# Kernel optimization log

Measured on AMD Instinct MI355X. Metric: run time of the kernel, lower is better.

Reference implementation:

```python
import jax, jax.numpy as jnp
import numpy as np

DIM, HEADS, DHEAD, CTX_DIM, FF_MULT = 320, 8, 40, 768, 4
INNER_FF = FF_MULT * DIM  # 1280
EPS = 1e-5


def layer_norm(x, g, b):
    mu = jnp.mean(x, axis=-1, keepdims=True)
    var = jnp.mean((x - mu) ** 2, axis=-1, keepdims=True)
    return (x - mu) * jax.lax.rsqrt(var + EPS) * g + b


def attention(x, ctx, wq, wk, wv, wo, bo):
    # x: [b, i, DIM], ctx: [b, j, c]
    b, i, _ = x.shape
    j = ctx.shape[1]
    q = (x @ wq).reshape(b, i, HEADS, DHEAD)
    k = (ctx @ wk).reshape(b, j, HEADS, DHEAD)
    v = (ctx @ wv).reshape(b, j, HEADS, DHEAD)
    scale = DHEAD ** -0.5
    sim = jnp.einsum('bihd,bjhd->bhij', q, k) * scale  # full NxN, non-flash
    attn = jax.nn.softmax(sim, axis=-1)
    out = jnp.einsum('bhij,bjhd->bihd', attn, v).reshape(b, i, HEADS * DHEAD)
    return out @ wo + bo


def setup_inputs() -> dict:
    key = jax.random.key(0)
    ks = jax.random.split(key, 24)
    nrm = lambda k, shp, fan: jax.random.normal(k, shp, jnp.float32) * (fan ** -0.5)
    d = {
        'x': jax.random.normal(ks[0], (1, 4096, DIM), jnp.float32),
        'context': jax.random.normal(ks[1], (1, 77, CTX_DIM), jnp.float32),
        'n1_g': jnp.ones((DIM,), jnp.float32), 'n1_b': jnp.zeros((DIM,), jnp.float32),
        'a1_wq': nrm(ks[2], (DIM, DIM), DIM), 'a1_wk': nrm(ks[3], (DIM, DIM), DIM),
        'a1_wv': nrm(ks[4], (DIM, DIM), DIM), 'a1_wo': nrm(ks[5], (DIM, DIM), DIM),
        'a1_bo': jnp.zeros((DIM,), jnp.float32),
        'n2_g': jnp.ones((DIM,), jnp.float32), 'n2_b': jnp.zeros((DIM,), jnp.float32),
        'a2_wq': nrm(ks[6], (DIM, DIM), DIM), 'a2_wk': nrm(ks[7], (CTX_DIM, DIM), CTX_DIM),
        'a2_wv': nrm(ks[8], (CTX_DIM, DIM), CTX_DIM), 'a2_wo': nrm(ks[9], (DIM, DIM), DIM),
        'a2_bo': jnp.zeros((DIM,), jnp.float32),
        'n3_g': jnp.ones((DIM,), jnp.float32), 'n3_b': jnp.zeros((DIM,), jnp.float32),
        'ff_w1': nrm(ks[10], (DIM, 2 * INNER_FF), DIM),
        'ff_b1': jnp.zeros((2 * INNER_FF,), jnp.float32),
        'ff_w2': nrm(ks[11], (INNER_FF, DIM), INNER_FF),
        'ff_b2': jnp.zeros((DIM,), jnp.float32),
    }
    return d


def reference(x, context, n1_g, n1_b, a1_wq, a1_wk, a1_wv, a1_wo, a1_bo,
              n2_g, n2_b, a2_wq, a2_wk, a2_wv, a2_wo, a2_bo,
              n3_g, n3_b, ff_w1, ff_b1, ff_w2, ff_b2):
    # self-attention
    x = attention(layer_norm(x, n1_g, n1_b), layer_norm(x, n1_g, n1_b),
                  a1_wq, a1_wk, a1_wv, a1_wo, a1_bo) + x
    # cross-attention with text context
    x = attention(layer_norm(x, n2_g, n2_b), context,
                  a2_wq, a2_wk, a2_wv, a2_wo, a2_bo) + x
    # GEGLU feed-forward
    h = layer_norm(x, n3_g, n3_b) @ ff_w1 + ff_b1
    val, gate = jnp.split(h, 2, axis=-1)
    x = (val * jax.nn.gelu(gate, approximate=False)) @ ff_w2 + ff_b2 + x
    return x
```

## Files before the change

kernel.cpp:

```cpp
#include <hip/hip_runtime.h>
#include <hip/hip_bf16.h>
#include <math.h>

typedef __bf16 bf16;
typedef __attribute__((ext_vector_type(8))) __bf16 bf16x8;
typedef __attribute__((ext_vector_type(4))) __bf16 bf16x4;
typedef __attribute__((ext_vector_type(4))) float f32x4;
typedef __attribute__((ext_vector_type(2))) float f32x2;
typedef __attribute__((ext_vector_type(4))) short shortx4;

#define NTOK 4096
#define DIM  320
#define HEADS 8
#define DHEAD 40
#define NCTX 77
#define CTXD 768
#define IFF  1280

#define QSCALE (0.15811388300841897f * 1.4426950408889634f)

__device__ __forceinline__ bf16x8 bzero8() {
    bf16x8 v;
#pragma unroll
    for (int e = 0; e < 8; ++e) v[e] = (bf16)0.0f;
    return v;
}

__device__ __forceinline__ void gld_lds16(const void* g, void* l) {
    __builtin_amdgcn_global_load_lds(
        (const __attribute__((address_space(1))) void*)g,
        (__attribute__((address_space(3))) void*)l, 16, 0, 0);
}

#define PRE_TILES 2280
#define CONV_BLOCKS 231

struct PreJob { const float* src; bf16* dst; int K, N, ntx, tile0, perm; };
struct PreTab { PreJob j[10]; };

__global__ __launch_bounds__(256)
void preprocess_all(PreTab P, const float* __restrict__ ctx, bf16* __restrict__ ctxb) {
    const int b = blockIdx.x;
    const int tx = threadIdx.x, ty = threadIdx.y;
    if (b >= PRE_TILES) {
        int i = (b - PRE_TILES) * 256 + ty * 32 + tx;
        if (i < NCTX * CTXD) ctxb[i] = (bf16)ctx[i];
        return;
    }
    int ji = 0;
#pragma unroll
    for (int k = 1; k < 10; ++k)
        if (b >= P.j[k].tile0) ji = k;
    const PreJob jb = P.j[ji];
    const int local = b - jb.tile0;
    const int n0 = (local % jb.ntx) * 32;
    const int k0 = (local / jb.ntx) * 32;

    __shared__ float tile[32][33];
#pragma unroll
    for (int i = 0; i < 4; ++i)
        tile[ty + i * 8][tx] = jb.src[(size_t)(k0 + ty + i * 8) * jb.N + n0 + tx];
    __syncthreads();
#pragma unroll
    for (int i = 0; i < 4; ++i) {
        int n = n0 + ty + i * 8;
        int nd = jb.perm ? ((n < 1280) ? 2 * n : 2 * (n - 1280) + 1) : n;
        jb.dst[(size_t)nd * jb.K + k0 + tx] = (bf16)tile[tx][ty + i * 8];
    }
}

__global__ __launch_bounds__(256)
void layernorm_kernel(const float* __restrict__ X, const float* __restrict__ g,
                      const float* __restrict__ b, bf16* __restrict__ Y) {
    int w = threadIdx.x >> 6, lane = threadIdx.x & 63;
    int row = blockIdx.x * 4 + w;
    const float* xr = X + (size_t)row * DIM;
    float v[5];
    float sum = 0.f;
#pragma unroll
    for (int c = 0; c < 5; ++c) { v[c] = xr[c * 64 + lane]; sum += v[c]; }
#pragma unroll
    for (int off = 1; off < 64; off <<= 1) sum += __shfl_xor(sum, off);
    float mu = sum * (1.f / 320.f);
    float vs = 0.f;
#pragma unroll
    for (int c = 0; c < 5; ++c) { float d = v[c] - mu; vs += d * d; }
#pragma unroll
    for (int off = 1; off < 64; off <<= 1) vs += __shfl_xor(vs, off);
    float rs = rsqrtf(vs * (1.f / 320.f) + 1e-5f);
    bf16* yr = Y + (size_t)row * DIM;
#pragma unroll
    for (int c = 0; c < 5; ++c)
        yr[c * 64 + lane] = (bf16)((v[c] - mu) * rs * g[c * 64 + lane] + b[c * 64 + lane]);
}

template <int EPI, int BM, int BN>
__global__ __launch_bounds__(256)
void gemm_db(const bf16* __restrict__ A, const bf16* __restrict__ Bt,
             int M, int N, int K,
             bf16* __restrict__ Y0, bf16* __restrict__ Y1, bf16* __restrict__ Y2,
             float* Yf, const float* __restrict__ bias, const float* res, int trs) {
    constexpr int ABYTES = BM * 128;
    constexpr int BBYTES = BN * 128;
    constexpr int FB = ABYTES + BBYTES;
    constexpr int WM = BM / 2;
    constexpr int WN = BN / 2;
    constexpr int MI = WM / 16;
    constexpr int NI = WN / 16;
    constexpr int ACH = BM / 32;
    constexpr int BCH = BN / 32;
    __shared__ char smem[2 * FB];
    const int t = threadIdx.x, lane = t & 63, w = t >> 6;
    const int wr = w >> 1, wc = w & 1;
    const int m0 = blockIdx.x * BM;
    const int n0 = blockIdx.y * BN;

    const bf16* asrc[ACH];
    const bf16* bsrc[BCH];
#pragma unroll
    for (int i = 0; i < ACH; ++i) {
        int ch = i * 256 + t;
        int row = ch >> 3, seg = (ch & 7) ^ (row & 7);
        asrc[i] = A + (size_t)(m0 + row) * K + seg * 8;
    }
#pragma unroll
    for (int i = 0; i < BCH; ++i) {
        int ch = i * 256 + t;
        int row = ch >> 3, seg = (ch & 7) ^ (row & 7);
        bsrc[i] = Bt + (size_t)(n0 + row) * K + seg * 8;
    }

    f32x4 acc[MI][NI];
#pragma unroll
    for (int mi = 0; mi < MI; ++mi)
#pragma unroll
        for (int ni = 0; ni < NI; ++ni)
#pragma unroll
            for (int r = 0; r < 4; ++r) acc[mi][ni][r] = 0.f;

    auto STAGE = [&](char* base, int k0) {
#pragma unroll
        for (int i = 0; i < ACH; ++i)
            gld_lds16(asrc[i] + k0, base + (i * 256 + w * 64) * 16);
#pragma unroll
        for (int i = 0; i < BCH; ++i)
            gld_lds16(bsrc[i] + k0, base + ABYTES + (i * 256 + w * 64) * 16);
    };

    char* cur = smem;
    char* nxt = smem + FB;
    STAGE(cur, 0);
    __syncthreads();

    for (int k0 = 0; k0 < K; k0 += 64) {
        if (k0 + 64 < K) STAGE(nxt, k0 + 64);
        bf16x8 a[MI][2], b[NI][2];
#pragma unroll
        for (int mi = 0; mi < MI; ++mi)
#pragma unroll
            for (int kh = 0; kh < 2; ++kh) {
                int row = wr * WM + mi * 16 + (lane & 15);
                a[mi][kh] = *(const bf16x8*)(cur + row * 128 +
                             ((kh * 64 + (lane >> 4) * 16) ^ ((row & 7) << 4)));
            }
#pragma unroll
        for (int ni = 0; ni < NI; ++ni)
#pragma unroll
            for (int kh = 0; kh < 2; ++kh) {
                int row = wc * WN + ni * 16 + (lane & 15);
                b[ni][kh] = *(const bf16x8*)(cur + ABYTES + row * 128 +
                             ((kh * 64 + (lane >> 4) * 16) ^ ((row & 7) << 4)));
            }
#pragma unroll
        for (int mi = 0; mi < MI; ++mi)
#pragma unroll
            for (int ni = 0; ni < NI; ++ni) {
                acc[mi][ni] = __builtin_amdgcn_mfma_f32_16x16x32_bf16(a[mi][0], b[ni][0], acc[mi][ni], 0, 0, 0);
                acc[mi][ni] = __builtin_amdgcn_mfma_f32_16x16x32_bf16(a[mi][1], b[ni][1], acc[mi][ni], 0, 0, 0);
            }
        __syncthreads();
        char* tmp = cur; cur = nxt; nxt = tmp;
    }

#pragma unroll
    for (int mi = 0; mi < MI; ++mi)
#pragma unroll
        for (int ni = 0; ni < NI; ++ni) {
            const int col = n0 + wc * WN + ni * 16 + (lane & 15);
            const int rowb = m0 + wr * WM + mi * 16 + (lane >> 4) * 4;
            if (EPI == 5) {
                if (col < 320) {
#pragma unroll
                    for (int r = 0; r < 4; ++r)
                        Y0[(size_t)(rowb + r) * 320 + col] = (bf16)(acc[mi][ni][r] * QSCALE);
                } else if (col < 640) {
#pragma unroll
                    for (int r = 0; r < 4; ++r)
                        Y1[(size_t)(rowb + r) * 320 + (col - 320)] = (bf16)acc[mi][ni][r];
                } else {
                    bf16x4 tv;
#pragma unroll
                    for (int r = 0; r < 4; ++r) tv[r] = (bf16)acc[mi][ni][r];
                    *(bf16x4*)(Y2 + (size_t)(col - 640) * trs + rowb) = tv;
                }
            } else if (EPI == 7) {
                int bidx = (col & 1) ? (1280 + (col >> 1)) : (col >> 1);
                float bc = bias[bidx];
#pragma unroll
                for (int r = 0; r < 4; ++r) {
                    float v = acc[mi][ni][r] + bc;
                    float other = __shfl_xor(v, 1);
                    if (!(col & 1)) {
                        float gl = 0.5f * other * (1.f + erff(other * 0.70710678118654752f));
                        Y0[(size_t)(rowb + r) * 1280 + (col >> 1)] = (bf16)(v * gl);
                    }
                }
            } else {
#pragma unroll
                for (int r = 0; r < 4; ++r) {
                    int row = rowb + r;
                    if (row < M) {
                        float v = acc[mi][ni][r];
                        if (EPI == 4) Y0[(size_t)row * N + col] = (bf16)(v * QSCALE);
                        else Yf[(size_t)row * N + col] = v + bias[col] + res[(size_t)row * N + col];
                    }
                }
            }
        }
}

__global__ __launch_bounds__(256)
void gemm_small6(const bf16* __restrict__ A, const bf16* __restrict__ Bt,
                 int M, int N, int K,
                 bf16* __restrict__ Y0, bf16* __restrict__ Y2, int trs) {
    __shared__ char smem[24 * 1024];
    const int t = threadIdx.x;
    const int lane = t & 63;
    const int w = t >> 6;
    const int wr = w >> 1, wc = w & 1;
    const int m0 = 0;
    const int n0 = blockIdx.y * 64;

    f32x4 acc[4][2];
#pragma unroll
    for (int mi = 0; mi < 4; ++mi)
#pragma unroll
        for (int ni = 0; ni < 2; ++ni)
#pragma unroll
            for (int r = 0; r < 4; ++r) acc[mi][ni][r] = 0.f;

    for (int k0 = 0; k0 < K; k0 += 64) {
#pragma unroll
        for (int i = 0; i < 4; ++i) {
            int c = t + i * 256;
            int row = c >> 3, seg = c & 7;
            int gr = m0 + row;
            bf16x8 v = bzero8();
            if (gr < M) v = *(const bf16x8*)(A + (size_t)gr * K + k0 + seg * 8);
            *(bf16x8*)(smem + row * 128 + ((seg * 16) ^ ((row & 7) << 4))) = v;
        }
#pragma unroll
        for (int i = 0; i < 2; ++i) {
            int c = t + i * 256;
            int row = c >> 3, seg = c & 7;
            bf16x8 v = *(const bf16x8*)(Bt + (size_t)(n0 + row) * K + k0 + seg * 8);
            *(bf16x8*)(smem + 16 * 1024 + row * 128 + ((seg * 16) ^ ((row & 7) << 4))) = v;
        }
        __syncthreads();

        bf16x8 a[4][2], bfr[2][2];
#pragma unroll
        for (int mi = 0; mi < 4; ++mi)
#pragma unroll
            for (int kh = 0; kh < 2; ++kh) {
                int row = wr * 64 + mi * 16 + (lane & 15);
                a[mi][kh] = *(const bf16x8*)(smem + row * 128 +
                             ((kh * 64 + (lane >> 4) * 16) ^ ((row & 7) << 4)));
            }
#pragma unroll
        for (int ni = 0; ni < 2; ++ni)
#pragma unroll
            for (int kh = 0; kh < 2; ++kh) {
                int row = wc * 32 + ni * 16 + (lane & 15);
                bfr[ni][kh] = *(const bf16x8*)(smem + 16 * 1024 + row * 128 +
                               ((kh * 64 + (lane >> 4) * 16) ^ ((row & 7) << 4)));
            }
#pragma unroll
        for (int mi = 0; mi < 4; ++mi)
#pragma unroll
            for (int ni = 0; ni < 2; ++ni) {
                acc[mi][ni] = __builtin_amdgcn_mfma_f32_16x16x32_bf16(a[mi][0], bfr[ni][0], acc[mi][ni], 0, 0, 0);
                acc[mi][ni] = __builtin_amdgcn_mfma_f32_16x16x32_bf16(a[mi][1], bfr[ni][1], acc[mi][ni], 0, 0, 0);
            }
        __syncthreads();
    }

#pragma unroll
    for (int mi = 0; mi < 4; ++mi)
#pragma unroll
        for (int ni = 0; ni < 2; ++ni) {
            const int col = n0 + wc * 32 + ni * 16 + (lane & 15);
            const int rowb = m0 + wr * 64 + mi * 16 + (lane >> 4) * 4;
            if (col < 320) {
#pragma unroll
                for (int r = 0; r < 4; ++r)
                    if (rowb + r < M) Y0[(size_t)(rowb + r) * 320 + col] = (bf16)acc[mi][ni][r];
            } else {
                bf16x4 tv;
#pragma unroll
                for (int r = 0; r < 4; ++r) tv[r] = (bf16)acc[mi][ni][r];
                *(bf16x4*)(Y2 + (size_t)(col - 320) * trs + rowb) = tv;
            }
        }
}

#define KVT 64
#define KBYTES 5120
#define VBYTES 6144
#define FBUF (KBYTES + VBYTES)

template <int DIRECT>
__global__ __launch_bounds__(256, 4)
void flash_attn5(const bf16* __restrict__ Qg, const bf16* __restrict__ Kg,
                 const bf16* __restrict__ VTg, bf16* __restrict__ O,
                 float* __restrict__ Opart, float* __restrict__ MLpart,
                 int nkv, int vstride, int tiles_per_split) {
    __shared__ char smem[2 * FBUF];
    const int t = threadIdx.x, lane = t & 63, w = t >> 6;
    const int g = lane >> 4, q = lane & 15;
    const int h = blockIdx.y, split = blockIdx.z;
    const int qb = blockIdx.x * 64 + w * 16;

    const int ntiles = (nkv + KVT - 1) / KVT;
    const int tt0 = split * tiles_per_split;
    int tt1 = tt0 + tiles_per_split;
    if (tt1 > ntiles) tt1 = ntiles;

    if (t < 128) {
        bf16x8 v = bzero8();
        if (((t & 63) >> 3) == 0) {
#pragma unroll
            for (int e = 0; e < 8; ++e) v[e] = (bf16)1.0f;
        }
        *(bf16x8*)(smem + (t >> 6) * FBUF + KBYTES + 5120 + (t & 63) * 16) = v;
    }

    const int nslot = (w == 3) ? 1 : 3;
    const bf16* srcp[3];
    int dstoff[3], sstep[3];
#pragma unroll
    for (int s = 0; s < 3; ++s) {
        int id = w * 3 + s;
        if (id < 5) {
            int c16 = id * 64 + lane;
            int row = c16 / 5, seg = c16 - row * 5;
            srcp[s] = Kg + (size_t)(tt0 * KVT + row) * DIM + h * DHEAD + seg * 8;
            sstep[s] = KVT * DIM;
            dstoff[s] = id * 1024;
        } else {
            int vv = id - 5;
            int c16 = vv * 64 + lane;
            int row = c16 >> 3, seg = (c16 & 7) ^ (row & 7);
            srcp[s] = VTg + (size_t)(h * DHEAD + row) * vstride + tt0 * KVT + seg * 8;
            sstep[s] = KVT;
            dstoff[s] = KBYTES + vv * 1024;
        }
    }

#define STAGE(BUFOFF)                                                     \
    do {                                                                  \
        _Pragma("unroll")                                                 \
        for (int s = 0; s < 3; ++s) {                                     \
            if (s < nslot) {                                              \
                gld_lds16(srcp[s], smem + (BUFOFF) + dstoff[s]);          \
                srcp[s] += sstep[s];                                      \
            }                                                             \
        }                                                                 \
    } while (0)

    bf16x8 qf0 = *(const bf16x8*)(Qg + (size_t)(qb + q) * DIM + h * DHEAD + g * 8);
    bf16x8 qf1 = bzero8();
    if (g == 0) qf1 = *(const bf16x8*)(Qg + (size_t)(qb + q) * DIM + h * DHEAD + 32);

    f32x4 accO[3];
#pragma unroll
    for (int dt = 0; dt < 3; ++dt)
#pragma unroll
        for (int r = 0; r < 4; ++r) accO[dt][r] = 0.f;
    float m_run = -1e30f;

#define TILE_BODY(KSC, J0)                                                        \
    do {                                                                          \
        const char* Ks_ = (KSC);                                                  \
        const char* Vs_ = Ks_ + KBYTES;                                           \
        f32x4 s4[4];                                                              \
        __builtin_amdgcn_s_setprio(1);                                            \
        _Pragma("unroll")                                                         \
        for (int jt = 0; jt < 4; ++jt) {                                          \
            const char* krow = Ks_ + (jt * 16 + q) * 80;                          \
            bf16x8 kb0 = *(const bf16x8*)(krow + g * 16);                         \
            bf16x8 kb1 = bzero8();                                                \
            if (g == 0) kb1 = *(const bf16x8*)(krow + 64);                        \
            f32x4 z;                                                              \
            _Pragma("unroll") for (int r = 0; r < 4; ++r) z[r] = 0.f;             \
            z = __builtin_amdgcn_mfma_f32_16x16x32_bf16(kb0, qf0, z, 0, 0, 0);    \
            z = __builtin_amdgcn_mfma_f32_16x16x32_bf16(kb1, qf1, z, 0, 0, 0);    \
            s4[jt] = z;                                                           \
        }                                                                         \
        __builtin_amdgcn_s_setprio(0);                                            \
        if ((J0) + KVT > nkv) {                                                   \
            _Pragma("unroll") for (int jt = 0; jt < 4; ++jt)                      \
            _Pragma("unroll") for (int r = 0; r < 4; ++r)                         \
                if ((J0) + jt * 16 + g * 4 + r >= nkv) s4[jt][r] = -1e30f;        \
        }                                                                         \
        f32x4 mvv = s4[0];                                                        \
        _Pragma("unroll") for (int jt = 1; jt < 4; ++jt)                          \
        _Pragma("unroll") for (int r = 0; r < 4; ++r)                             \
            mvv[r] = fmaxf(mvv[r], s4[jt][r]);                                    \
        float mt = fmaxf(fmaxf(mvv[0], mvv[1]), fmaxf(mvv[2], mvv[3]));           \
        mt = fmaxf(mt, __shfl_xor(mt, 16));                                       \
        mt = fmaxf(mt, __shfl_xor(mt, 32));                                       \
        if (!__all(mt <= m_run + 8.f)) {                                          \
            float mnew = fmaxf(m_run, mt);                                        \
            float f = exp2f(m_run - mnew);                                        \
            m_run = mnew;                                                         \
            _Pragma("unroll") for (int dt = 0; dt < 3; ++dt)                      \
            _Pragma("unroll") for (int r = 0; r < 4; ++r) accO[dt][r] *= f;       \
        }                                                                         \
        union PU { bf16x4 hv; shortx4 sv; } pk[4];                                \
        _Pragma("unroll") for (int jt = 0; jt < 4; ++jt) {                        \
            bf16x4 hv;                                                            \
            _Pragma("unroll") for (int r = 0; r < 4; ++r)                         \
                hv[r] = (bf16)exp2f(s4[jt][r] - m_run);                           \
            pk[jt].hv = hv;                                                       \
        }                                                                         \
        __builtin_amdgcn_s_setprio(1);                                            \
        _Pragma("unroll") for (int dt = 0; dt < 3; ++dt) {                        \
            const char* vrow = Vs_ + (dt * 16 + q) * 128;                         \
            _Pragma("unroll") for (int jt = 0; jt < 4; ++jt) {                    \
                shortx4 vb = *(const shortx4*)(vrow +                             \
                               ((jt * 32 + g * 8) ^ ((q & 7) << 4)));             \
                accO[dt] = __builtin_amdgcn_mfma_f32_16x16x16bf16_1k(             \
                               vb, pk[jt].sv, accO[dt], 0, 0, 0);                 \
            }                                                                     \
        }                                                                         \
        __builtin_amdgcn_s_setprio(0);                                            \
        __syncthreads();                                                          \
    } while (0)

    STAGE(0);
    __syncthreads();

    int tt = tt0;
    while (tt < tt1) {
        if (tt + 1 < tt1) STAGE(FBUF);
        TILE_BODY(smem, tt * KVT);
        ++tt;
        if (tt >= tt1) break;
        if (tt + 1 < tt1) STAGE(0);
        TILE_BODY(smem + FBUF, tt * KVT);
        ++tt;
    }
#undef TILE_BODY
#undef STAGE

    float l = __shfl(accO[2][0], 32 + q);

    if (DIRECT) {
        float inv = 1.f / l;
#pragma unroll
        for (int dt = 0; dt < 3; ++dt) {
            if (dt < 2 || g < 2) {
                bf16x4 o;
#pragma unroll
                for (int r = 0; r < 4; ++r) o[r] = (bf16)(accO[dt][r] * inv);
                *(bf16x4*)(O + (size_t)(qb + q) * DIM + h * DHEAD + dt * 16 + g * 4) = o;
            }
        }
    } else {
        size_t rowi = (size_t)(split * HEADS + h) * NTOK + qb + q;
#pragma unroll
        for (int dt = 0; dt < 3; ++dt) {
            if (dt < 2 || g < 2)
                *(f32x4*)(Opart + rowi * 40 + dt * 16 + g * 4) = accO[dt];
        }
        if (g == 2) {
            f32x2 ml;
            ml[0] = m_run; ml[1] = accO[2][0];
            *(f32x2*)(MLpart + rowi * 2) = ml;
        }
    }
}

__global__ __launch_bounds__(256)
void flash_combine(const float* __restrict__ Opart, const float* __restrict__ MLpart,
                   bf16* __restrict__ O) {
    int idx = blockIdx.x * 256 + threadIdx.x;
    int qi = idx / 40, c = idx - qi * 40;
    int h = c / 5, c8 = c - h * 5;
    float mv[4], lv[4];
    float M = -1e30f;
#pragma unroll
    for (int s = 0; s < 4; ++s) {
        f32x2 ml = *(const f32x2*)(MLpart + ((size_t)(s * HEADS + h) * NTOK + qi) * 2);
        mv[s] = ml[0]; lv[s] = ml[1];
        M = fmaxf(M, ml[0]);
    }
    float wgt[4], denom = 0.f;
#pragma unroll
    for (int s = 0; s < 4; ++s) { wgt[s] = exp2f(mv[s] - M); denom += wgt[s] * lv[s]; }
    float inv = 1.f / denom;
    float o[8];
#pragma unroll
    for (int e = 0; e < 8; ++e) o[e] = 0.f;
#pragma unroll
    for (int s = 0; s < 4; ++s) {
        const float* op = Opart + ((size_t)(s * HEADS + h) * NTOK + qi) * 40 + c8 * 8;
#pragma unroll
        for (int e = 0; e < 8; ++e) o[e] += wgt[s] * op[e];
    }
    bf16x8 ov;
#pragma unroll
    for (int e = 0; e < 8; ++e) ov[e] = (bf16)(o[e] * inv);
    *(bf16x8*)(O + (size_t)qi * DIM + h * DHEAD + c8 * 8) = ov;
}

extern "C" void kernel_launch(void* const* d_in, const int* in_sizes, int n_in,
                              void* d_out, int out_size, void* d_ws, size_t ws_size,
                              hipStream_t stream) {
    const float* x     = (const float*)d_in[0];
    const float* ctx   = (const float*)d_in[1];
    const float* n1_g  = (const float*)d_in[2];
    const float* n1_b  = (const float*)d_in[3];
    const float* a1_wq = (const float*)d_in[4];
    const float* a1_wk = (const float*)d_in[5];
    const float* a1_wv = (const float*)d_in[6];
    const float* a1_wo = (const float*)d_in[7];
    const float* a1_bo = (const float*)d_in[8];
    const float* n2_g  = (const float*)d_in[9];
    const float* n2_b  = (const float*)d_in[10];
    const float* a2_wq = (const float*)d_in[11];
    const float* a2_wk = (const float*)d_in[12];
    const float* a2_wv = (const float*)d_in[13];
    const float* a2_wo = (const float*)d_in[14];
    const float* a2_bo = (const float*)d_in[15];
    const float* n3_g  = (const float*)d_in[16];
    const float* n3_b  = (const float*)d_in[17];
    const float* ff_w1 = (const float*)d_in[18];
    const float* ff_b1 = (const float*)d_in[19];
    const float* ff_w2 = (const float*)d_in[20];
    const float* ff_b2 = (const float*)d_in[21];

    char* ws = (char*)d_ws;
    size_t off = 0;
    auto alloc = [&](size_t bytes) -> char* {
        char* p = ws + off;
        off += (bytes + 255) & ~(size_t)255;
        return p;
    };
    bf16* lnbuf  = (bf16*)alloc((size_t)NTOK * DIM * 2);
    bf16* qbuf   = (bf16*)alloc((size_t)NTOK * DIM * 2);
    bf16* kbuf   = (bf16*)alloc((size_t)NTOK * DIM * 2);
    bf16* vtbuf  = (bf16*)alloc((size_t)DIM * NTOK * 2);
    bf16* abuf   = (bf16*)alloc((size_t)NTOK * DIM * 2);
    bf16* hbuf   = (bf16*)alloc((size_t)NTOK * 2 * IFF * 2);
    bf16* gbuf   = (bf16*)alloc((size_t)NTOK * IFF * 2);
    bf16* ctxb   = (bf16*)alloc((size_t)NCTX * CTXD * 2);
    bf16* k2buf  = (bf16*)alloc((size_t)128 * DIM * 2);
    bf16* vt2buf = (bf16*)alloc((size_t)DIM * 128 * 2);
    bf16* wqkvT  = (bf16*)alloc((size_t)960 * DIM * 2);
    bf16* woT    = (bf16*)alloc((size_t)DIM * DIM * 2);
    bf16* q2T    = (bf16*)alloc((size_t)DIM * DIM * 2);
    bf16* wkv2T  = (bf16*)alloc((size_t)640 * CTXD * 2);
    bf16* o2T    = (bf16*)alloc((size_t)DIM * DIM * 2);
    bf16* w1T    = (bf16*)alloc((size_t)2 * IFF * DIM * 2);
    bf16* w2T    = (bf16*)alloc((size_t)IFF * DIM * 2);
    float* out   = (float*)d_out;

    float* Opart  = (float*)hbuf;
    float* MLpart = (float*)gbuf;

    {
        PreTab P;
        auto set = [&](int i, const float* s, bf16* d, int K, int N, int tile0, int perm) {
            P.j[i].src = s; P.j[i].dst = d; P.j[i].K = K; P.j[i].N = N;
            P.j[i].ntx = N / 32; P.j[i].tile0 = tile0; P.j[i].perm = perm;
        };
        set(0, a1_wq, wqkvT,                        320, 320,    0, 0);
        set(1, a1_wk, wqkvT + (size_t)320 * 320,    320, 320,  100, 0);
        set(2, a1_wv, wqkvT + (size_t)640 * 320,    320, 320,  200, 0);
        set(3, a1_wo, woT,                          320, 320,  300, 0);
        set(4, a2_wq, q2T,                          320, 320,  400, 0);
        set(5, a2_wo, o2T,                          320, 320,  500, 0);
        set(6, a2_wk, wkv2T,                        768, 320,  600, 0);
        set(7, a2_wv, wkv2T + (size_t)320 * 768,    768, 320,  840, 0);
        set(8, ff_w1, w1T,                          320, 2560, 1080, 1);
        set(9, ff_w2, w2T,                          1280, 320, 1880, 0);
        preprocess_all<<<PRE_TILES + CONV_BLOCKS, dim3(32, 8), 0, stream>>>(P, ctx, ctxb);
    }

    layernorm_kernel<<<1024, 256, 0, stream>>>(x, n1_g, n1_b, lnbuf);
    gemm_db<5, 128, 64><<<dim3(32, 15), 256, 0, stream>>>(lnbuf, wqkvT, NTOK, 960, DIM,
                                                          qbuf, kbuf, vtbuf, nullptr, nullptr, nullptr, NTOK);
    flash_attn5<0><<<dim3(64, 8, 4), 256, 0, stream>>>(qbuf, kbuf, vtbuf, nullptr,
                                                       Opart, MLpart, NTOK, NTOK, 16);
    flash_combine<<<640, 256, 0, stream>>>(Opart, MLpart, abuf);
    gemm_db<2, 64, 64><<<dim3(64, 5), 256, 0, stream>>>(abuf, woT, NTOK, DIM, DIM,
                                                        nullptr, nullptr, nullptr, out, a1_bo, x, 0);

    layernorm_kernel<<<1024, 256, 0, stream>>>(out, n2_g, n2_b, lnbuf);
    gemm_db<4, 64, 64><<<dim3(64, 5), 256, 0, stream>>>(lnbuf, q2T, NTOK, DIM, DIM,
                                                        qbuf, nullptr, nullptr, nullptr, nullptr, nullptr, 0);
    gemm_small6<<<dim3(1, 10), 256, 0, stream>>>(ctxb, wkv2T, NCTX, 640, CTXD,
                                                 k2buf, vt2buf, 128);
    flash_attn5<1><<<dim3(64, 8, 1), 256, 0, stream>>>(qbuf, k2buf, vt2buf, abuf,
                                                       nullptr, nullptr, NCTX, 128, 2);
    gemm_db<2, 64, 64><<<dim3(64, 5), 256, 0, stream>>>(abuf, o2T, NTOK, DIM, DIM,
                                                        nullptr, nullptr, nullptr, out, a2_bo, out, 0);

    layernorm_kernel<<<1024, 256, 0, stream>>>(out, n3_g, n3_b, lnbuf);
    gemm_db<7, 128, 128><<<dim3(32, 20), 256, 0, stream>>>(lnbuf, w1T, NTOK, 2 * IFF, DIM,
                                                           gbuf, nullptr, nullptr, nullptr, ff_b1, nullptr, 0);
    gemm_db<2, 64, 64><<<dim3(64, 5), 256, 0, stream>>>(gbuf, w2T, NTOK, DIM, IFF,
                                                        nullptr, nullptr, nullptr, out, ff_b2, out, 0);
}
```

Baseline: 200.9 us.

## Swizzle GEMM block order, merge LN2 with cross-attn KV GEMM, retile FF1

Adds an XCD-aware block-id swizzle to every gemm_db launch so consecutive blocks are spread across chiplets, improving L2 locality. Merges the second layernorm and the small context K/V projection into one launch, dropping a kernel launch and letting the tiny GEMM overlap the layernorm. Also changes the FF1 GEMM tile from 128x128 to 128x64, doubling its grid for better occupancy and CU balance. The swizzle assumes the block count divides by 8, and the FF1 retile trades data reuse for more parallelism.

```diff
diff --git a/kernel.cpp b/kernel.cpp
--- a/kernel.cpp
+++ b/kernel.cpp
@@ -69,32 +69,36 @@
     }
 }
 
+__device__ __forceinline__ void ln_body(const float* __restrict__ X, const float* __restrict__ g,
+                                        const float* __restrict__ b, bf16* __restrict__ Y, int row) {
+    int lane = threadIdx.x & 63;
+    const float* xr = X + (size_t)row * DIM;
+    float v[5];
+    float sum = 0.f;
+#pragma unroll
+    for (int c = 0; c < 5; ++c) { v[c] = xr[c * 64 + lane]; sum += v[c]; }
+#pragma unroll
+    for (int off = 1; off < 64; off <<= 1) sum += __shfl_xor(sum, off);
+    float mu = sum * (1.f / 320.f);
+    float vs = 0.f;
+#pragma unroll
+    for (int c = 0; c < 5; ++c) { float d = v[c] - mu; vs += d * d; }
+#pragma unroll
+    for (int off = 1; off < 64; off <<= 1) vs += __shfl_xor(vs, off);
+    float rs = rsqrtf(vs * (1.f / 320.f) + 1e-5f);
+    bf16* yr = Y + (size_t)row * DIM;
+#pragma unroll
+    for (int c = 0; c < 5; ++c)
+        yr[c * 64 + lane] = (bf16)((v[c] - mu) * rs * g[c * 64 + lane] + b[c * 64 + lane]);
+}
+
 __global__ __launch_bounds__(256)
 void layernorm_kernel(const float* __restrict__ X, const float* __restrict__ g,
                       const float* __restrict__ b, bf16* __restrict__ Y) {
-    int w = threadIdx.x >> 6, lane = threadIdx.x & 63;
-    int row = blockIdx.x * 4 + w;
-    const float* xr = X + (size_t)row * DIM;
-    float v[5];
-    float sum = 0.f;
-#pragma unroll
-    for (int c = 0; c < 5; ++c) { v[c] = xr[c * 64 + lane]; sum += v[c]; }
-#pragma unroll
-    for (int off = 1; off < 64; off <<= 1) sum += __shfl_xor(sum, off);
-    float mu = sum * (1.f / 320.f);
-    float vs = 0.f;
-#pragma unroll
-    for (int c = 0; c < 5; ++c) { float d = v[c] - mu; vs += d * d; }
-#pragma unroll
-    for (int off = 1; off < 64; off <<= 1) vs += __shfl_xor(vs, off);
-    float rs = rsqrtf(vs * (1.f / 320.f) + 1e-5f);
-    bf16* yr = Y + (size_t)row * DIM;
-#pragma unroll
-    for (int c = 0; c < 5; ++c)
-        yr[c * 64 + lane] = (bf16)((v[c] - mu) * rs * g[c * 64 + lane] + b[c * 64 + lane]);
-}
-
-template <int EPI, int BM, int BN>
+    ln_body(X, g, b, Y, blockIdx.x * 4 + (threadIdx.x >> 6));
+}
+
+template <int EPI, int BM, int BN, int SWZ>
 __global__ __launch_bounds__(256)
 void gemm_db(const bf16* __restrict__ A, const bf16* __restrict__ Bt,
              int M, int N, int K,
@@ -112,8 +116,17 @@
     __shared__ char smem[2 * FB];
     const int t = threadIdx.x, lane = t & 63, w = t >> 6;
     const int wr = w >> 1, wc = w & 1;
-    const int m0 = blockIdx.x * BM;
-    const int n0 = blockIdx.y * BN;
+
+    int bx = blockIdx.x, by = blockIdx.y;
+    if (SWZ) {
+        int gx = gridDim.x;
+        int nwg = gx * gridDim.y;
+        int bid = by * gx + bx;
+        int s = (bid & 7) * (nwg >> 3) + (bid >> 3);
+        bx = s % gx; by = s / gx;
+    }
+    const int m0 = bx * BM;
+    const int n0 = by * BN;
 
     const bf16* asrc[ACH];
     const bf16* bsrc[BCH];
@@ -230,16 +243,21 @@
 }
 
 __global__ __launch_bounds__(256)
-void gemm_small6(const bf16* __restrict__ A, const bf16* __restrict__ Bt,
-                 int M, int N, int K,
-                 bf16* __restrict__ Y0, bf16* __restrict__ Y2, int trs) {
+void ln2_plus_cross(const float* __restrict__ X, const float* __restrict__ g,
+                    const float* __restrict__ bb, bf16* __restrict__ Y,
+                    const bf16* __restrict__ A, const bf16* __restrict__ Bt,
+                    bf16* __restrict__ Y0, bf16* __restrict__ Y2, int trs) {
     __shared__ char smem[24 * 1024];
+    if (blockIdx.x < 1024) {
+        ln_body(X, g, bb, Y, blockIdx.x * 4 + (threadIdx.x >> 6));
+        return;
+    }
+    const int M = NCTX, K = CTXD;
     const int t = threadIdx.x;
     const int lane = t & 63;
     const int w = t >> 6;
     const int wr = w >> 1, wc = w & 1;
-    const int m0 = 0;
-    const int n0 = blockIdx.y * 64;
+    const int n0 = (blockIdx.x - 1024) * 64;
 
     f32x4 acc[4][2];
 #pragma unroll
@@ -254,9 +272,8 @@
         for (int i = 0; i < 4; ++i) {
             int c = t + i * 256;
             int row = c >> 3, seg = c & 7;
-            int gr = m0 + row;
             bf16x8 v = bzero8();
-            if (gr < M) v = *(const bf16x8*)(A + (size_t)gr * K + k0 + seg * 8);
+            if (row < M) v = *(const bf16x8*)(A + (size_t)row * K + k0 + seg * 8);
             *(bf16x8*)(smem + row * 128 + ((seg * 16) ^ ((row & 7) << 4))) = v;
         }
 #pragma unroll
@@ -300,7 +317,7 @@
 #pragma unroll
         for (int ni = 0; ni < 2; ++ni) {
             const int col = n0 + wc * 32 + ni * 16 + (lane & 15);
-            const int rowb = m0 + wr * 64 + mi * 16 + (lane >> 4) * 4;
+            const int rowb = wr * 64 + mi * 16 + (lane >> 4) * 4;
             if (col < 320) {
 #pragma unroll
                 for (int r = 0; r < 4; ++r)
@@ -600,27 +617,26 @@
     }
 
     layernorm_kernel<<<1024, 256, 0, stream>>>(x, n1_g, n1_b, lnbuf);
-    gemm_db<5, 128, 64><<<dim3(32, 15), 256, 0, stream>>>(lnbuf, wqkvT, NTOK, 960, DIM,
-                                                          qbuf, kbuf, vtbuf, nullptr, nullptr, nullptr, NTOK);
+    gemm_db<5, 128, 64, 1><<<dim3(32, 15), 256, 0, stream>>>(lnbuf, wqkvT, NTOK, 960, DIM,
+                                                             qbuf, kbuf, vtbuf, nullptr, nullptr, nullptr, NTOK);
     flash_attn5<0><<<dim3(64, 8, 4), 256, 0, stream>>>(qbuf, kbuf, vtbuf, nullptr,
                                                        Opart, MLpart, NTOK, NTOK, 16);
     flash_combine<<<640, 256, 0, stream>>>(Opart, MLpart, abuf);
-    gemm_db<2, 64, 64><<<dim3(64, 5), 256, 0, stream>>>(abuf, woT, NTOK, DIM, DIM,
-                                                        nullptr, nullptr, nullptr, out, a1_bo, x, 0);
-
-    layernorm_kernel<<<1024, 256, 0, stream>>>(out, n2_g, n2_b, lnbuf);
-    gemm_db<4, 64, 64><<<dim3(64, 5), 256, 0, stream>>>(lnbuf, q2T, NTOK, DIM, DIM,
-                                                        qbuf, nullptr, nullptr, nullptr, nullptr, nullptr, 0);
-    gemm_small6<<<dim3(1, 10), 256, 0, stream>>>(ctxb, wkv2T, NCTX, 640, CTXD,
-                                                 k2buf, vt2buf, 128);
+    gemm_db<2, 64, 64, 1><<<dim3(64, 5), 256, 0, stream>>>(abuf, woT, NTOK, DIM, DIM,
+                                                           nullptr, nullptr, nullptr, out, a1_bo, x, 0);
+
+    ln2_plus_cross<<<1034, 256, 0, stream>>>(out, n2_g, n2_b, lnbuf,
+                                             ctxb, wkv2T, k2buf, vt2buf, 128);
+    gemm_db<4, 64, 64, 1><<<dim3(64, 5), 256, 0, stream>>>(lnbuf, q2T, NTOK, DIM, DIM,
+                                                           qbuf, nullptr, nullptr, nullptr, nullptr, nullptr, 0);
     flash_attn5<1><<<dim3(64, 8, 1), 256, 0, stream>>>(qbuf, k2buf, vt2buf, abuf,
                                                        nullptr, nullptr, NCTX, 128, 2);
-    gemm_db<2, 64, 64><<<dim3(64, 5), 256, 0, stream>>>(abuf, o2T, NTOK, DIM, DIM,
-                                                        nullptr, nullptr, nullptr, out, a2_bo, out, 0);
+    gemm_db<2, 64, 64, 1><<<dim3(64, 5), 256, 0, stream>>>(abuf, o2T, NTOK, DIM, DIM,
+                                                           nullptr, nullptr, nullptr, out, a2_bo, out, 0);
 
     layernorm_kernel<<<1024, 256, 0, stream>>>(out, n3_g, n3_b, lnbuf);
-    gemm_db<7, 128, 128><<<dim3(32, 20), 256, 0, stream>>>(lnbuf, w1T, NTOK, 2 * IFF, DIM,
-                                                           gbuf, nullptr, nullptr, nullptr, ff_b1, nullptr, 0);
-    gemm_db<2, 64, 64><<<dim3(64, 5), 256, 0, stream>>>(gbuf, w2T, NTOK, DIM, IFF,
-                                                        nullptr, nullptr, nullptr, out, ff_b2, out, 0);
-}
+    gemm_db<7, 128, 64, 1><<<dim3(32, 40), 256, 0, stream>>>(lnbuf, w1T, NTOK, 2 * IFF, DIM,
+                                                             gbuf, nullptr, nullptr, nullptr, ff_b1, nullptr, 0);
+    gemm_db<2, 64, 64, 1><<<dim3(64, 5), 256, 0, stream>>>(gbuf, w2T, NTOK, DIM, IFF,
+                                                           nullptr, nullptr, nullptr, out, ff_b2, out, 0);
+}
```

Result: faster. 187.2 us (-6.8%).
